# Performance work log

Measured on AMD Instinct MI355X. Metric: run time of the kernel, lower is better.

Reference implementation:

```python
import jax, jax.numpy as jnp
import numpy as np

EPS = 1e-5
B, M, N, D = 8, 4096, 1024, 1024


def setup_inputs() -> dict:
    key = jax.random.key(0)
    kx, kw, kb, kg, kbe = jax.random.split(key, 5)
    return {
        "x": jax.random.normal(kx, (B, M, N), dtype=jnp.float32),
        "w": jax.random.normal(kw, (N, D), dtype=jnp.float32) * 0.02,
        "b": jax.random.normal(kb, (D,), dtype=jnp.float32) * 0.02,
        "gamma": jax.random.uniform(kg, (N,), dtype=jnp.float32, minval=0.5, maxval=1.5),
        "beta": jax.random.normal(kbe, (N,), dtype=jnp.float32) * 0.02,
    }


def reference(x, w, b, gamma, beta):
    # Fused LayerNorm (over last dim, biased variance, eps=1e-5) + matmul + bias.
    mean = jnp.mean(x, axis=-1, keepdims=True)                 # [B,M,1]
    var = jnp.mean(jnp.square(x - mean), axis=-1, keepdims=True)
    rstd = jax.lax.rsqrt(var + EPS)                            # [B,M,1]
    ln = (x - mean) * rstd * gamma + beta                      # [B,M,N]
    return jnp.einsum('bmn,nd->bmd', ln, w) + b                # [B,M,D]
```

## Files before the change

### kernel.cpp

```cpp
#include <hip/hip_runtime.h>
#include <stdint.h>

#define RROWS 32768
#define KDIM  1024
#define DDIM  1024

typedef __bf16 bf16;
typedef __bf16 bf16x4 __attribute__((ext_vector_type(4)));
typedef __bf16 bf16x8 __attribute__((ext_vector_type(8)));
typedef float  f32x4  __attribute__((ext_vector_type(4)));

typedef __attribute__((address_space(1))) const unsigned int* gas_ptr;
typedef __attribute__((address_space(3))) unsigned int* las_ptr;

__global__ __launch_bounds__(256) void prep_gt(const float* __restrict__ w,
                                               const float* __restrict__ gamma,
                                               bf16* __restrict__ Gt) {
    __shared__ float tile[64][65];
    const int k0 = blockIdx.x * 64;
    const int d0 = blockIdx.y * 64;
    const int t  = threadIdx.x;
    const int col4 = (t & 15) * 4;
    const int rowb = t >> 4;
#pragma unroll
    for (int r = 0; r < 4; ++r) {
        const int k = rowb + r * 16;
        const float4 v = *(const float4*)&w[(size_t)(k0 + k) * DDIM + d0 + col4];
        const float g = gamma[k0 + k];
        tile[k][col4 + 0] = v.x * g;
        tile[k][col4 + 1] = v.y * g;
        tile[k][col4 + 2] = v.z * g;
        tile[k][col4 + 3] = v.w * g;
    }
    __syncthreads();
#pragma unroll
    for (int r = 0; r < 2; ++r) {
        const int d  = (t >> 3) + r * 32;
        const int ks = (t & 7) * 8;
        bf16x8 o;
#pragma unroll
        for (int j = 0; j < 8; ++j) o[j] = (bf16)tile[ks + j][d];
        *(bf16x8*)&Gt[(size_t)(d0 + d) * KDIM + k0 + ks] = o;
    }
}

__global__ __launch_bounds__(256) void prep_part(const float* __restrict__ w,
                                                 const float* __restrict__ gamma,
                                                 const float* __restrict__ beta,
                                                 float* __restrict__ partG,
                                                 float* __restrict__ partB) {
    const int d  = blockIdx.x * 256 + threadIdx.x;
    const int kc = blockIdx.y;
    float ag = 0.f, ab = 0.f;
    for (int k = kc * 64; k < kc * 64 + 64; ++k) {
        const float wv = w[(size_t)k * DDIM + d];
        ag += gamma[k] * wv;
        ab += beta[k] * wv;
    }
    partG[(size_t)kc * DDIM + d] = ag;
    partB[(size_t)kc * DDIM + d] = ab;
}

__global__ __launch_bounds__(256) void prep_reduce(const float* __restrict__ partG,
                                                   const float* __restrict__ partB,
                                                   const float* __restrict__ b,
                                                   float* __restrict__ gw,
                                                   float* __restrict__ cvec) {
    const int d = blockIdx.x * 256 + threadIdx.x;
    float g = 0.f, a = 0.f;
#pragma unroll
    for (int j = 0; j < 16; ++j) {
        g += partG[(size_t)j * DDIM + d];
        a += partB[(size_t)j * DDIM + d];
    }
    gw[d]   = g;
    cvec[d] = a + b[d];
}

__global__ __launch_bounds__(256) void ln_convert(const float* __restrict__ x,
                                                  bf16* __restrict__ xb) {
    const int wave = threadIdx.x >> 6;
    const int lane = threadIdx.x & 63;
    const int row  = blockIdx.x * 4 + wave;
    const float4* xr = (const float4*)(x + (size_t)row * KDIM);

    float4 v[4];
    float s1 = 0.f, s2 = 0.f;
#pragma unroll
    for (int j = 0; j < 4; ++j) {
        v[j] = xr[lane + j * 64];
        s1 += v[j].x + v[j].y + v[j].z + v[j].w;
        s2 += v[j].x * v[j].x + v[j].y * v[j].y + v[j].z * v[j].z + v[j].w * v[j].w;
    }
#pragma unroll
    for (int ofs = 1; ofs < 64; ofs <<= 1) {
        s1 += __shfl_xor(s1, ofs, 64);
        s2 += __shfl_xor(s2, ofs, 64);
    }
    const float mean = s1 * (1.0f / KDIM);
    const float var  = s2 * (1.0f / KDIM) - mean * mean;
    const float rstd = rsqrtf(var + 1e-5f);

    bf16x4* xo = (bf16x4*)(xb + (size_t)row * KDIM);
#pragma unroll
    for (int j = 0; j < 4; ++j) {
        bf16x4 o;
        o[0] = (bf16)((v[j].x - mean) * rstd);
        o[1] = (bf16)((v[j].y - mean) * rstd);
        o[2] = (bf16)((v[j].z - mean) * rstd);
        o[3] = (bf16)((v[j].w - mean) * rstd);
        xo[lane + j * 64] = o;
    }
}

__device__ __forceinline__ void stage_half(const bf16* __restrict__ g0,
                                           bf16* lregion, int kt, int h, int tid) {
#pragma unroll
    for (int j = 0; j < 2; ++j) {
        const int ci = j * 512 + tid;
        const int r  = ci >> 2;
        const int qs = (ci & 3) ^ (r & 3);
        const bf16* gp = g0 + (size_t)r * KDIM + kt * 64 + h * 32 + qs * 8;
        char* lp = (char*)lregion + ci * 16;
        __builtin_amdgcn_global_load_lds((gas_ptr)(const void*)gp,
                                         (las_ptr)(void*)lp, 16, 0, 0);
    }
}

__device__ __forceinline__ bf16x8 ld_frag(const bf16* region, int r, int g) {
    return *(const bf16x8*)(region + r * 32 + ((g ^ (r & 3)) * 8));
}

#define MFMA_QUAD(MOFF)                                                         \
    __builtin_amdgcn_s_setprio(1);                                              \
    _Pragma("unroll")                                                           \
    for (int m_ = 0; m_ < 4; ++m_) {                                            \
        _Pragma("unroll")                                                       \
        for (int n_ = 0; n_ < 4; ++n_)                                          \
            acc[(MOFF) + m_][n_] = __builtin_amdgcn_mfma_f32_16x16x32_bf16(     \
                af[m_], bfr[n_], acc[(MOFF) + m_][n_], 0, 0, 0);                \
    }                                                                           \
    __builtin_amdgcn_s_setprio(0);

__global__ __launch_bounds__(512, 2) void gemm256(const bf16* __restrict__ xb,
                                                  const bf16* __restrict__ Gt,
                                                  const float* __restrict__ cvec,
                                                  float* __restrict__ out) {
    __shared__ __align__(16) bf16 As[2][2][8192];
    __shared__ __align__(16) bf16 Bs[2][2][8192];

    const int tid  = threadIdx.x;
    const int bid  = blockIdx.x;
    const int wg   = (bid & 7) * 64 + (bid >> 3);
    const int mT   = wg >> 2;
    const int dT   = wg & 3;
    const int row0 = mT * 256;
    const int col0 = dT * 256;

    const int wave = tid >> 6;
    const int lane = tid & 63;
    const int wm   = wave >> 2;
    const int wn   = wave & 3;
    const int r16  = lane & 15;
    const int g    = lane >> 4;

    const bf16* aG = xb + (size_t)row0 * KDIM;
    const bf16* bG = Gt + (size_t)col0 * KDIM;

    f32x4 acc[8][4];
#pragma unroll
    for (int m = 0; m < 8; ++m)
#pragma unroll
        for (int n = 0; n < 4; ++n) acc[m][n] = (f32x4)0.0f;

    stage_half(aG, &As[0][0][0], 0, 0, tid);
    stage_half(bG, &Bs[0][0][0], 0, 0, tid);
    stage_half(aG, &As[0][1][0], 0, 1, tid);
    stage_half(bG, &Bs[0][1][0], 0, 1, tid);
    asm volatile("s_waitcnt vmcnt(4)" ::: "memory");
    __builtin_amdgcn_s_barrier();

    bf16x8 af[4], bfr[4];
    for (int t = 0; t < 16; ++t) {
        const int  c  = t & 1;
        const int  o  = c ^ 1;
        const bool st = (t < 15);
        const bf16* A0 = &As[c][0][0];
        const bf16* A1 = &As[c][1][0];
        const bf16* B0 = &Bs[c][0][0];
        const bf16* B1 = &Bs[c][1][0];
        const int am = wm * 128 + r16;
        const int bn = wn * 64 + r16;

#pragma unroll
        for (int m = 0; m < 4; ++m) af[m] = ld_frag(A0, am + m * 16, g);
#pragma unroll
        for (int n = 0; n < 4; ++n) bfr[n] = ld_frag(B0, bn + n * 16, g);
        if (st) stage_half(aG, &As[o][0][0], t + 1, 0, tid);
        __builtin_amdgcn_s_barrier();
        MFMA_QUAD(0)
        __builtin_amdgcn_s_barrier();

#pragma unroll
        for (int m = 0; m < 4; ++m) af[m] = ld_frag(A0, am + 64 + m * 16, g);
        if (st) {
            stage_half(bG, &Bs[o][0][0], t + 1, 0, tid);
            asm volatile("s_waitcnt vmcnt(4)" ::: "memory");
        } else {
            asm volatile("s_waitcnt vmcnt(0)" ::: "memory");
        }
        __builtin_amdgcn_s_barrier();
        MFMA_QUAD(4)
        __builtin_amdgcn_s_barrier();

#pragma unroll
        for (int m = 0; m < 4; ++m) af[m] = ld_frag(A1, am + m * 16, g);
#pragma unroll
        for (int n = 0; n < 4; ++n) bfr[n] = ld_frag(B1, bn + n * 16, g);
        if (st) stage_half(aG, &As[o][1][0], t + 1, 1, tid);
        __builtin_amdgcn_s_barrier();
        MFMA_QUAD(0)
        __builtin_amdgcn_s_barrier();

#pragma unroll
        for (int m = 0; m < 4; ++m) af[m] = ld_frag(A1, am + 64 + m * 16, g);
        if (st) {
            stage_half(bG, &Bs[o][1][0], t + 1, 1, tid);
            asm volatile("s_waitcnt vmcnt(4)" ::: "memory");
        }
        __builtin_amdgcn_s_barrier();
        MFMA_QUAD(4)
        __builtin_amdgcn_s_barrier();
    }

#pragma unroll
    for (int n = 0; n < 4; ++n) {
        const int colL = wn * 64 + n * 16 + r16;
        const float cv = cvec[col0 + colL];
#pragma unroll
        for (int m = 0; m < 8; ++m) {
#pragma unroll
            for (int rg = 0; rg < 4; ++rg) {
                const int rowL = wm * 128 + m * 16 + g * 4 + rg;
                out[(size_t)(row0 + rowL) * DDIM + col0 + colL] = acc[m][n][rg] + cv;
            }
        }
    }
}

#define BM 128
#define BN 128
#define FBK 32
#define APAD 40

__global__ __launch_bounds__(256) void fused_gemm(const float* __restrict__ x,
                                                  const bf16* __restrict__ Gt,
                                                  const float* __restrict__ gw,
                                                  const float* __restrict__ cvec,
                                                  float* __restrict__ out) {
    __shared__ __align__(16) bf16 As2[BM * APAD];
    __shared__ __align__(16) bf16 Bs2[BM * FBK];
    __shared__ float meanS[BM];
    __shared__ float rstdS[BM];

    const int t     = threadIdx.x;
    const int mTile = blockIdx.x;
    const int dTile = blockIdx.y;
    const int row0  = mTile * BM;
    const int col0  = dTile * BN;
    const int wave = t >> 6;
    const int lane = t & 63;
    const int wr   = wave >> 1;
    const int wc   = wave & 1;
    const int a_row = t >> 3;
    const int a_seg = t & 7;

    float s1[4] = {0.f, 0.f, 0.f, 0.f};
    float s2[4] = {0.f, 0.f, 0.f, 0.f};
    f32x4 acc[4][4];
#pragma unroll
    for (int i = 0; i < 4; ++i)
#pragma unroll
        for (int j = 0; j < 4; ++j) acc[i][j] = (f32x4)0.0f;

    for (int k0 = 0; k0 < KDIM; k0 += FBK) {
        __syncthreads();
#pragma unroll
        for (int j = 0; j < 2; ++j) {
            const int off  = j * 4096 + t * 16;
            const int brow = off >> 6;
            const int kseg = (off & 63) >> 1;
            const bf16* gp = Gt + (size_t)(col0 + brow) * KDIM + k0 + kseg;
            char* lp = (char*)Bs2 + off;
            __builtin_amdgcn_global_load_lds((gas_ptr)(const void*)gp,
                                             (las_ptr)(void*)lp, 16, 0, 0);
        }
#pragma unroll
        for (int r = 0; r < 4; ++r) {
            const int row = r * 32 + a_row;
            const float4 v = *(const float4*)&x[(size_t)(row0 + row) * KDIM + k0 + a_seg * 4];
            s1[r] += v.x + v.y + v.z + v.w;
            s2[r] += v.x * v.x + v.y * v.y + v.z * v.z + v.w * v.w;
            bf16x4 pk;
            pk[0] = (bf16)v.x; pk[1] = (bf16)v.y; pk[2] = (bf16)v.z; pk[3] = (bf16)v.w;
            *(bf16x4*)&As2[row * APAD + a_seg * 4] = pk;
        }
        __syncthreads();

        bf16x8 af[4], bfr[4];
        const int arow = wr * 64 + (lane & 15);
        const int brow = wc * 64 + (lane & 15);
        const int koff = (lane >> 4) * 8;
#pragma unroll
        for (int i = 0; i < 4; ++i)
            af[i] = *(const bf16x8*)&As2[(arow + i * 16) * APAD + koff];
#pragma unroll
        for (int j = 0; j < 4; ++j)
            bfr[j] = *(const bf16x8*)&Bs2[(brow + j * 16) * FBK + koff];
#pragma unroll
        for (int i = 0; i < 4; ++i)
#pragma unroll
            for (int j = 0; j < 4; ++j)
                acc[i][j] = __builtin_amdgcn_mfma_f32_16x16x32_bf16(af[i], bfr[j], acc[i][j], 0, 0, 0);
    }

#pragma unroll
    for (int r = 0; r < 4; ++r) {
        float a = s1[r], b = s2[r];
#pragma unroll
        for (int ofs = 1; ofs < 8; ofs <<= 1) {
            a += __shfl_xor(a, ofs, 64);
            b += __shfl_xor(b, ofs, 64);
        }
        if (a_seg == 0) {
            const int row = r * 32 + a_row;
            const float mean = a * (1.0f / KDIM);
            const float var  = b * (1.0f / KDIM) - mean * mean;
            meanS[row] = mean;
            rstdS[row] = rsqrtf(var + 1e-5f);
        }
    }
    __syncthreads();

    const int lr = (lane >> 4) * 4;
    const int lc = lane & 15;
#pragma unroll
    for (int j = 0; j < 4; ++j) {
        const int col = col0 + wc * 64 + j * 16 + lc;
        const float gwv = gw[col];
        const float cv  = cvec[col];
#pragma unroll
        for (int i = 0; i < 4; ++i) {
#pragma unroll
            for (int rg = 0; rg < 4; ++rg) {
                const int rowL = wr * 64 + i * 16 + lr + rg;
                const float vv = rstdS[rowL] * (acc[i][j][rg] - meanS[rowL] * gwv) + cv;
                out[(size_t)(row0 + rowL) * DDIM + col] = vv;
            }
        }
    }
}

extern "C" void kernel_launch(void* const* d_in, const int* in_sizes, int n_in,
                              void* d_out, int out_size, void* d_ws, size_t ws_size,
                              hipStream_t stream) {
    const float* x     = (const float*)d_in[0];
    const float* w     = (const float*)d_in[1];
    const float* b     = (const float*)d_in[2];
    const float* gamma = (const float*)d_in[3];
    const float* beta  = (const float*)d_in[4];
    float* out = (float*)d_out;

    char* ws = (char*)d_ws;
    const size_t XB_B = (size_t)RROWS * KDIM * sizeof(bf16);
    bf16*  xb    = (bf16*)ws;
    bf16*  Gt    = (bf16*)(ws + XB_B);
    float* partG = (float*)(ws + XB_B + (2u << 20));
    float* partB = (float*)(ws + XB_B + (2u << 20) + (64u << 10));
    float* gw    = (float*)(ws + XB_B + (2u << 20) + (128u << 10));
    float* cvec  = (float*)(ws + XB_B + (2u << 20) + (132u << 10));

    const bool big_ws = ws_size >= XB_B + (3u << 20);

    if (big_ws) {
        prep_gt<<<dim3(16, 16), 256, 0, stream>>>(w, gamma, Gt);
        prep_part<<<dim3(4, 16), 256, 0, stream>>>(w, gamma, beta, partG, partB);
        prep_reduce<<<4, 256, 0, stream>>>(partG, partB, b, gw, cvec);
        ln_convert<<<RROWS / 4, 256, 0, stream>>>(x, xb);
        gemm256<<<dim3(512), 512, 0, stream>>>(xb, Gt, cvec, out);
    } else {
        bf16*  Gt2    = (bf16*)ws;
        float* partG2 = (float*)(ws + (2u << 20));
        float* partB2 = (float*)(ws + (2u << 20) + (64u << 10));
        float* gw2    = (float*)(ws + (2u << 20) + (128u << 10));
        float* cvec2  = (float*)(ws + (2u << 20) + (132u << 10));
        prep_gt<<<dim3(16, 16), 256, 0, stream>>>(w, gamma, Gt2);
        prep_part<<<dim3(4, 16), 256, 0, stream>>>(w, gamma, beta, partG2, partB2);
        prep_reduce<<<4, 256, 0, stream>>>(partG2, partB2, b, gw2, cvec2);
        fused_gemm<<<dim3(256, 8), 256, 0, stream>>>(x, Gt2, gw2, cvec2, out);
    }
}
```

Baseline: 337.2 us.

## Restructure gemm256 LDS staging into row-halves with full-K fragments and interleaved waves

The shared-memory tiles change from two K-halves of 32 to two row-halves holding the full 64-wide K slice, with an 8-way XOR swizzle. Each wave now loads fragments for both K sub-steps and issues 2x4x2 MFMA quadrants in an order that reuses A and B fragments across phases, with per-wave rows and columns interleaved. The loop runs 15 pipelined iterations plus a peeled final one, and the vmcnt waits are reordered. The aim is to cut redundant LDS fragment loads and overlap global-to-LDS staging with MFMA work better, at the cost of more fragment registers and more complex wait logic.

```diff
diff --git a/kernel.cpp b/kernel.cpp
--- a/kernel.cpp
+++ b/kernel.cpp
@@ -114,40 +114,45 @@
 }
 
 __device__ __forceinline__ void stage_half(const bf16* __restrict__ g0,
-                                           bf16* lregion, int kt, int h, int tid) {
+                                           bf16* lhalf, int kt, int rowOff, int tid) {
 #pragma unroll
     for (int j = 0; j < 2; ++j) {
         const int ci = j * 512 + tid;
-        const int r  = ci >> 2;
-        const int qs = (ci & 3) ^ (r & 3);
-        const bf16* gp = g0 + (size_t)r * KDIM + kt * 64 + h * 32 + qs * 8;
-        char* lp = (char*)lregion + ci * 16;
+        const int rl = ci >> 3;
+        const int q  = (ci & 7) ^ (rl & 7);
+        const bf16* gp = g0 + (size_t)(rowOff + rl) * KDIM + kt * 64 + q * 8;
+        char* lp = (char*)lhalf + ci * 16;
         __builtin_amdgcn_global_load_lds((gas_ptr)(const void*)gp,
                                          (las_ptr)(void*)lp, 16, 0, 0);
     }
 }
 
-__device__ __forceinline__ bf16x8 ld_frag(const bf16* region, int r, int g) {
-    return *(const bf16x8*)(region + r * 32 + ((g ^ (r & 3)) * 8));
-}
-
-#define MFMA_QUAD(MOFF)                                                         \
-    __builtin_amdgcn_s_setprio(1);                                              \
-    _Pragma("unroll")                                                           \
-    for (int m_ = 0; m_ < 4; ++m_) {                                            \
-        _Pragma("unroll")                                                       \
-        for (int n_ = 0; n_ < 4; ++n_)                                          \
-            acc[(MOFF) + m_][n_] = __builtin_amdgcn_mfma_f32_16x16x32_bf16(     \
-                af[m_], bfr[n_], acc[(MOFF) + m_][n_], 0, 0, 0);                \
-    }                                                                           \
+__device__ __forceinline__ bf16x8 ld_frag(const bf16* base, int row, int qk) {
+    return *(const bf16x8*)(base + row * 64 + (qk ^ (row & 7)) * 8);
+}
+
+#define MFMA_Q(MO, NO, AFR, BFR)                                               \
+    __builtin_amdgcn_s_setprio(1);                                             \
+    _Pragma("unroll")                                                          \
+    for (int kk_ = 0; kk_ < 2; ++kk_) {                                        \
+        _Pragma("unroll")                                                      \
+        for (int mm_ = 0; mm_ < 4; ++mm_) {                                    \
+            _Pragma("unroll")                                                  \
+            for (int nn_ = 0; nn_ < 2; ++nn_)                                  \
+                acc[(MO) + mm_][(NO) + nn_] =                                  \
+                    __builtin_amdgcn_mfma_f32_16x16x32_bf16(                   \
+                        AFR[mm_][kk_], BFR[nn_][kk_],                          \
+                        acc[(MO) + mm_][(NO) + nn_], 0, 0, 0);                 \
+        }                                                                      \
+    }                                                                          \
     __builtin_amdgcn_s_setprio(0);
 
 __global__ __launch_bounds__(512, 2) void gemm256(const bf16* __restrict__ xb,
                                                   const bf16* __restrict__ Gt,
                                                   const float* __restrict__ cvec,
                                                   float* __restrict__ out) {
-    __shared__ __align__(16) bf16 As[2][2][8192];
-    __shared__ __align__(16) bf16 Bs[2][2][8192];
+    __shared__ __align__(16) bf16 As[2][256 * 64];
+    __shared__ __align__(16) bf16 Bs[2][256 * 64];
 
     const int tid  = threadIdx.x;
     const int bid  = blockIdx.x;
@@ -173,76 +178,122 @@
 #pragma unroll
         for (int n = 0; n < 4; ++n) acc[m][n] = (f32x4)0.0f;
 
-    stage_half(aG, &As[0][0][0], 0, 0, tid);
-    stage_half(bG, &Bs[0][0][0], 0, 0, tid);
-    stage_half(aG, &As[0][1][0], 0, 1, tid);
-    stage_half(bG, &Bs[0][1][0], 0, 1, tid);
+    stage_half(aG, &As[0][0],        0, 0,   tid);
+    stage_half(bG, &Bs[0][0],        0, 0,   tid);
+    stage_half(bG, &Bs[0][128 * 64], 0, 128, tid);
+    stage_half(aG, &As[0][128 * 64], 0, 128, tid);
     asm volatile("s_waitcnt vmcnt(4)" ::: "memory");
     __builtin_amdgcn_s_barrier();
 
-    bf16x8 af[4], bfr[4];
-    for (int t = 0; t < 16; ++t) {
-        const int  c  = t & 1;
-        const int  o  = c ^ 1;
-        const bool st = (t < 15);
-        const bf16* A0 = &As[c][0][0];
-        const bf16* A1 = &As[c][1][0];
-        const bf16* B0 = &Bs[c][0][0];
-        const bf16* B1 = &Bs[c][1][0];
-        const int am = wm * 128 + r16;
-        const int bn = wn * 64 + r16;
-
-#pragma unroll
-        for (int m = 0; m < 4; ++m) af[m] = ld_frag(A0, am + m * 16, g);
-#pragma unroll
-        for (int n = 0; n < 4; ++n) bfr[n] = ld_frag(B0, bn + n * 16, g);
-        if (st) stage_half(aG, &As[o][0][0], t + 1, 0, tid);
-        __builtin_amdgcn_s_barrier();
-        MFMA_QUAD(0)
-        __builtin_amdgcn_s_barrier();
-
-#pragma unroll
-        for (int m = 0; m < 4; ++m) af[m] = ld_frag(A0, am + 64 + m * 16, g);
-        if (st) {
-            stage_half(bG, &Bs[o][0][0], t + 1, 0, tid);
-            asm volatile("s_waitcnt vmcnt(4)" ::: "memory");
-        } else {
-            asm volatile("s_waitcnt vmcnt(0)" ::: "memory");
-        }
-        __builtin_amdgcn_s_barrier();
-        MFMA_QUAD(4)
-        __builtin_amdgcn_s_barrier();
-
-#pragma unroll
-        for (int m = 0; m < 4; ++m) af[m] = ld_frag(A1, am + m * 16, g);
-#pragma unroll
-        for (int n = 0; n < 4; ++n) bfr[n] = ld_frag(B1, bn + n * 16, g);
-        if (st) stage_half(aG, &As[o][1][0], t + 1, 1, tid);
-        __builtin_amdgcn_s_barrier();
-        MFMA_QUAD(0)
-        __builtin_amdgcn_s_barrier();
-
-#pragma unroll
-        for (int m = 0; m < 4; ++m) af[m] = ld_frag(A1, am + 64 + m * 16, g);
-        if (st) {
-            stage_half(bG, &Bs[o][1][0], t + 1, 1, tid);
-            asm volatile("s_waitcnt vmcnt(4)" ::: "memory");
-        }
-        __builtin_amdgcn_s_barrier();
-        MFMA_QUAD(4)
-        __builtin_amdgcn_s_barrier();
+    bf16x8 af[4][2], bl[2][2], bh[2][2];
+
+#pragma unroll 1
+    for (int t = 0; t < 15; ++t) {
+        const int c = t & 1;
+        const int o = c ^ 1;
+        const bf16* Ac = &As[c][0];
+        const bf16* Bc = &Bs[c][0];
+
+#pragma unroll
+        for (int m = 0; m < 4; ++m) {
+            const int r = m * 32 + wm * 16 + r16;
+#pragma unroll
+            for (int kk = 0; kk < 2; ++kk) af[m][kk] = ld_frag(Ac, r, kk * 4 + g);
+        }
+#pragma unroll
+        for (int n = 0; n < 2; ++n) {
+            const int r = n * 64 + wn * 16 + r16;
+#pragma unroll
+            for (int kk = 0; kk < 2; ++kk) bl[n][kk] = ld_frag(Bc, r, kk * 4 + g);
+        }
+        stage_half(aG, &As[o][0], t + 1, 0, tid);
+        asm volatile("s_waitcnt vmcnt(4)" ::: "memory");
+        __builtin_amdgcn_s_barrier();
+        MFMA_Q(0, 0, af, bl)
+        __builtin_amdgcn_s_barrier();
+
+#pragma unroll
+        for (int n = 0; n < 2; ++n) {
+            const int r = (n + 2) * 64 + wn * 16 + r16;
+#pragma unroll
+            for (int kk = 0; kk < 2; ++kk) bh[n][kk] = ld_frag(Bc, r, kk * 4 + g);
+        }
+        stage_half(bG, &Bs[o][0], t + 1, 0, tid);
+        asm volatile("s_waitcnt vmcnt(4)" ::: "memory");
+        __builtin_amdgcn_s_barrier();
+        MFMA_Q(0, 2, af, bh)
+        __builtin_amdgcn_s_barrier();
+
+#pragma unroll
+        for (int m = 0; m < 4; ++m) {
+            const int r = (m + 4) * 32 + wm * 16 + r16;
+#pragma unroll
+            for (int kk = 0; kk < 2; ++kk) af[m][kk] = ld_frag(Ac, r, kk * 4 + g);
+        }
+        stage_half(bG, &Bs[o][128 * 64], t + 1, 128, tid);
+        __builtin_amdgcn_s_barrier();
+        MFMA_Q(4, 2, af, bh)
+        __builtin_amdgcn_s_barrier();
+
+        stage_half(aG, &As[o][128 * 64], t + 1, 128, tid);
+        asm volatile("s_waitcnt vmcnt(4)" ::: "memory");
+        __builtin_amdgcn_s_barrier();
+        MFMA_Q(4, 0, af, bl)
+        __builtin_amdgcn_s_barrier();
+    }
+
+    {
+        const bf16* Ac = &As[1][0];
+        const bf16* Bc = &Bs[1][0];
+#pragma unroll
+        for (int m = 0; m < 4; ++m) {
+            const int r = m * 32 + wm * 16 + r16;
+#pragma unroll
+            for (int kk = 0; kk < 2; ++kk) af[m][kk] = ld_frag(Ac, r, kk * 4 + g);
+        }
+#pragma unroll
+        for (int n = 0; n < 2; ++n) {
+            const int r = n * 64 + wn * 16 + r16;
+#pragma unroll
+            for (int kk = 0; kk < 2; ++kk) bl[n][kk] = ld_frag(Bc, r, kk * 4 + g);
+        }
+        asm volatile("s_waitcnt vmcnt(2)" ::: "memory");
+        __builtin_amdgcn_s_barrier();
+        MFMA_Q(0, 0, af, bl)
+        __builtin_amdgcn_s_barrier();
+
+#pragma unroll
+        for (int n = 0; n < 2; ++n) {
+            const int r = (n + 2) * 64 + wn * 16 + r16;
+#pragma unroll
+            for (int kk = 0; kk < 2; ++kk) bh[n][kk] = ld_frag(Bc, r, kk * 4 + g);
+        }
+        asm volatile("s_waitcnt vmcnt(0)" ::: "memory");
+        __builtin_amdgcn_s_barrier();
+        MFMA_Q(0, 2, af, bh)
+        __builtin_amdgcn_s_barrier();
+
+#pragma unroll
+        for (int m = 0; m < 4; ++m) {
+            const int r = (m + 4) * 32 + wm * 16 + r16;
+#pragma unroll
+            for (int kk = 0; kk < 2; ++kk) af[m][kk] = ld_frag(Ac, r, kk * 4 + g);
+        }
+        __builtin_amdgcn_s_barrier();
+        MFMA_Q(4, 2, af, bh)
+        MFMA_Q(4, 0, af, bl)
     }
 
 #pragma unroll
     for (int n = 0; n < 4; ++n) {
-        const int colL = wn * 64 + n * 16 + r16;
+        const int colL = n * 64 + wn * 16 + r16;
         const float cv = cvec[col0 + colL];
 #pragma unroll
         for (int m = 0; m < 8; ++m) {
+            const int rbase = m * 32 + wm * 16 + g * 4;
 #pragma unroll
             for (int rg = 0; rg < 4; ++rg) {
-                const int rowL = wm * 128 + m * 16 + g * 4 + rg;
-                out[(size_t)(row0 + rowL) * DDIM + col0 + colL] = acc[m][n][rg] + cv;
+                out[(size_t)(row0 + rbase + rg) * DDIM + col0 + colL] = acc[m][n][rg] + cv;
             }
         }
     }
```

New measurement: 315.8 us. 6.4% less time.

## Replace half-tile ping-pong schedule with full-tile double buffer in GEMM

Applied to the files above, without the earlier changes.

The 256x256 bf16 GEMM now stages a whole 64-wide K tile per buffer with an 8-way XOR swizzle, instead of two 32-wide halves with a 4-way swizzle. The main loop uses a single __syncthreads per K step, prefetches the next tile, and then runs all MFMAs for the current tile. This replaces the old schedule of eight barriers per step, fine-grained vmcnt waits and setprio bracketing. The aim is to cut barrier overhead and make the loop simpler. In exchange it relies on the implicit wait inside __syncthreads and may overlap global loads with MFMA work less finely.

```diff
diff --git a/kernel.cpp b/kernel.cpp
--- a/kernel.cpp
+++ b/kernel.cpp
@@ -113,41 +113,30 @@
     }
 }
 
-__device__ __forceinline__ void stage_half(const bf16* __restrict__ g0,
-                                           bf16* lregion, int kt, int h, int tid) {
-#pragma unroll
-    for (int j = 0; j < 2; ++j) {
+__device__ __forceinline__ void stage_tile(const bf16* __restrict__ g0,
+                                           bf16* lbuf, int kt, int tid) {
+#pragma unroll
+    for (int j = 0; j < 4; ++j) {
         const int ci = j * 512 + tid;
-        const int r  = ci >> 2;
-        const int qs = (ci & 3) ^ (r & 3);
-        const bf16* gp = g0 + (size_t)r * KDIM + kt * 64 + h * 32 + qs * 8;
-        char* lp = (char*)lregion + ci * 16;
+        const int r  = ci >> 3;
+        const int q  = (ci & 7) ^ (r & 7);
+        const bf16* gp = g0 + (size_t)r * KDIM + kt * 64 + q * 8;
+        char* lp = (char*)lbuf + ci * 16;
         __builtin_amdgcn_global_load_lds((gas_ptr)(const void*)gp,
                                          (las_ptr)(void*)lp, 16, 0, 0);
     }
 }
 
-__device__ __forceinline__ bf16x8 ld_frag(const bf16* region, int r, int g) {
-    return *(const bf16x8*)(region + r * 32 + ((g ^ (r & 3)) * 8));
-}
-
-#define MFMA_QUAD(MOFF)                                                         \
-    __builtin_amdgcn_s_setprio(1);                                              \
-    _Pragma("unroll")                                                           \
-    for (int m_ = 0; m_ < 4; ++m_) {                                            \
-        _Pragma("unroll")                                                       \
-        for (int n_ = 0; n_ < 4; ++n_)                                          \
-            acc[(MOFF) + m_][n_] = __builtin_amdgcn_mfma_f32_16x16x32_bf16(     \
-                af[m_], bfr[n_], acc[(MOFF) + m_][n_], 0, 0, 0);                \
-    }                                                                           \
-    __builtin_amdgcn_s_setprio(0);
+__device__ __forceinline__ bf16x8 ld_frag(const bf16* base, int row, int qk) {
+    return *(const bf16x8*)(base + row * 64 + (qk ^ (row & 7)) * 8);
+}
 
 __global__ __launch_bounds__(512, 2) void gemm256(const bf16* __restrict__ xb,
                                                   const bf16* __restrict__ Gt,
                                                   const float* __restrict__ cvec,
                                                   float* __restrict__ out) {
-    __shared__ __align__(16) bf16 As[2][2][8192];
-    __shared__ __align__(16) bf16 Bs[2][2][8192];
+    __shared__ __align__(16) bf16 As[2][256 * 64];
+    __shared__ __align__(16) bf16 Bs[2][256 * 64];
 
     const int tid  = threadIdx.x;
     const int bid  = blockIdx.x;
@@ -173,64 +162,39 @@
 #pragma unroll
         for (int n = 0; n < 4; ++n) acc[m][n] = (f32x4)0.0f;
 
-    stage_half(aG, &As[0][0][0], 0, 0, tid);
-    stage_half(bG, &Bs[0][0][0], 0, 0, tid);
-    stage_half(aG, &As[0][1][0], 0, 1, tid);
-    stage_half(bG, &Bs[0][1][0], 0, 1, tid);
-    asm volatile("s_waitcnt vmcnt(4)" ::: "memory");
-    __builtin_amdgcn_s_barrier();
-
-    bf16x8 af[4], bfr[4];
+    stage_tile(aG, &As[0][0], 0, tid);
+    stage_tile(bG, &Bs[0][0], 0, tid);
+
+#pragma unroll 1
     for (int t = 0; t < 16; ++t) {
-        const int  c  = t & 1;
-        const int  o  = c ^ 1;
-        const bool st = (t < 15);
-        const bf16* A0 = &As[c][0][0];
-        const bf16* A1 = &As[c][1][0];
-        const bf16* B0 = &Bs[c][0][0];
-        const bf16* B1 = &Bs[c][1][0];
-        const int am = wm * 128 + r16;
-        const int bn = wn * 64 + r16;
-
-#pragma unroll
-        for (int m = 0; m < 4; ++m) af[m] = ld_frag(A0, am + m * 16, g);
-#pragma unroll
-        for (int n = 0; n < 4; ++n) bfr[n] = ld_frag(B0, bn + n * 16, g);
-        if (st) stage_half(aG, &As[o][0][0], t + 1, 0, tid);
-        __builtin_amdgcn_s_barrier();
-        MFMA_QUAD(0)
-        __builtin_amdgcn_s_barrier();
-
-#pragma unroll
-        for (int m = 0; m < 4; ++m) af[m] = ld_frag(A0, am + 64 + m * 16, g);
-        if (st) {
-            stage_half(bG, &Bs[o][0][0], t + 1, 0, tid);
-            asm volatile("s_waitcnt vmcnt(4)" ::: "memory");
-        } else {
-            asm volatile("s_waitcnt vmcnt(0)" ::: "memory");
-        }
-        __builtin_amdgcn_s_barrier();
-        MFMA_QUAD(4)
-        __builtin_amdgcn_s_barrier();
-
-#pragma unroll
-        for (int m = 0; m < 4; ++m) af[m] = ld_frag(A1, am + m * 16, g);
-#pragma unroll
-        for (int n = 0; n < 4; ++n) bfr[n] = ld_frag(B1, bn + n * 16, g);
-        if (st) stage_half(aG, &As[o][1][0], t + 1, 1, tid);
-        __builtin_amdgcn_s_barrier();
-        MFMA_QUAD(0)
-        __builtin_amdgcn_s_barrier();
-
-#pragma unroll
-        for (int m = 0; m < 4; ++m) af[m] = ld_frag(A1, am + 64 + m * 16, g);
-        if (st) {
-            stage_half(bG, &Bs[o][1][0], t + 1, 1, tid);
-            asm volatile("s_waitcnt vmcnt(4)" ::: "memory");
-        }
-        __builtin_amdgcn_s_barrier();
-        MFMA_QUAD(4)
-        __builtin_amdgcn_s_barrier();
+        const int c = t & 1;
+        __syncthreads();
+        if (t < 15) {
+            stage_tile(aG, &As[c ^ 1][0], t + 1, tid);
+            stage_tile(bG, &Bs[c ^ 1][0], t + 1, tid);
+        }
+        const bf16* Ac = &As[c][0];
+        const bf16* Bc = &Bs[c][0];
+
+        bf16x8 bfr[4][2];
+#pragma unroll
+        for (int n = 0; n < 4; ++n) {
+            const int r = wn * 64 + n * 16 + r16;
+#pragma unroll
+            for (int kk = 0; kk < 2; ++kk) bfr[n][kk] = ld_frag(Bc, r, kk * 4 + g);
+        }
+#pragma unroll
+        for (int m = 0; m < 8; ++m) {
+            const int r = wm * 128 + m * 16 + r16;
+            const bf16x8 a0 = ld_frag(Ac, r, g);
+            const bf16x8 a1 = ld_frag(Ac, r, 4 + g);
+#pragma unroll
+            for (int n = 0; n < 4; ++n)
+                acc[m][n] = __builtin_amdgcn_mfma_f32_16x16x32_bf16(a0, bfr[n][0], acc[m][n], 0, 0, 0);
+#pragma unroll
+            for (int n = 0; n < 4; ++n)
+                acc[m][n] = __builtin_amdgcn_mfma_f32_16x16x32_bf16(a1, bfr[n][1], acc[m][n], 0, 0, 0);
+        }
     }
 
 #pragma unroll
@@ -239,10 +203,10 @@
         const float cv = cvec[col0 + colL];
 #pragma unroll
         for (int m = 0; m < 8; ++m) {
+            const int rbase = wm * 128 + m * 16 + g * 4;
 #pragma unroll
             for (int rg = 0; rg < 4; ++rg) {
-                const int rowL = wm * 128 + m * 16 + g * 4 + rg;
-                out[(size_t)(row0 + rowL) * DDIM + col0 + colL] = acc[m][n][rg] + cv;
+                out[(size_t)(row0 + rbase + rg) * DDIM + col0 + colL] = acc[m][n][rg] + cv;
             }
         }
     }
```

After: 329.4 us. 1.02x faster.
